# Performance work log

Measured on AMD Instinct MI355X. Metric: run time of the kernel, lower is better.

## Reference

```python
import jax, jax.numpy as jnp
import numpy as np

NGROUP, CIN, COUT, K, HIDDEN = 8, 16, 16, 5, True


def _build_mask():
    # Group-causal PixelCNN-style mask for a 5x5 kernel.
    # Spatial: rows above center fully visible; center row visible left of center.
    # Center tap: input group g_in visible to output group g_out iff
    #   g_in <= g_out (hidden layer) or g_in < g_out (input layer).
    nout, cinall = NGROUP * COUT, NGROUP * CIN
    c = K // 2
    m = np.zeros((nout, cinall, K, K), dtype=np.float32)
    m[:, :, :c, :] = 1.0          # rows strictly above center
    m[:, :, c, :c] = 1.0          # center row, left of center
    g_out = np.arange(nout)[:, None] // COUT   # (nout,1)
    g_in = np.arange(cinall)[None, :] // CIN   # (1,cinall)
    center_ok = (g_in <= g_out) if HIDDEN else (g_in < g_out)
    m[:, :, c, c] = center_ok.astype(np.float32)
    return jnp.asarray(m)

_MASK = _build_mask()


def setup_inputs() -> dict:
    key = jax.random.key(0)
    k1, k2 = jax.random.split(key)
    x = jax.random.normal(k1, (8, 128, 256, 512), dtype=jnp.float32)
    weight = jax.random.uniform(k2, (128, 128, 5, 5), dtype=jnp.float32)
    bias = jnp.zeros((128,), dtype=jnp.float32)
    slope = jnp.zeros((128,), dtype=jnp.float32)  # PReLU slope (zero -> ReLU)
    return {"x": x, "weight": weight, "bias": bias, "slope": slope}


def reference(x, weight, bias, slope):
    w = weight * _MASK  # apply causal group mask
    # context pad by 2 then valid 5x5 conv == SAME padding conv
    y = jax.lax.conv_general_dilated(
        x, w, window_strides=(1, 1), padding=((2, 2), (2, 2)),
        dimension_numbers=("NCHW", "OIHW", "NCHW"))
    y = y + bias[None, :, None, None]
    a = slope[None, :, None, None]
    return jnp.where(y > 0, y, a * y)  # per-channel PReLU
```

## Files before the change

kernel.cpp:

```cpp
#include <hip/hip_runtime.h>
#include <hip/hip_bf16.h>

typedef __attribute__((ext_vector_type(8))) short short8;
typedef __attribute__((ext_vector_type(4))) float f32x4;

#define CH 128
#define H 256
#define W 512
#define PH 258
#define PW 516
#define NTAPS 13
#define P_BYTES (PH * PW * CH * 2)
#define P_SHORTS (PH * PW * CH)
#define CHW (CH * H * W)

#define GRAN_PER_ROW 544
#define NLOADS 34
#define TILE_SHORTS (4 * GRAN_PER_ROW * 8)
#define ROW_SHORTS (GRAN_PER_ROW * 8)

#define GLD_LDS16(g, l)                                                        \
  __builtin_amdgcn_global_load_lds(                                            \
      (const __attribute__((address_space(1))) void*)(g),                      \
      (__attribute__((address_space(3))) void*)(l), 16, 0, 0)

__global__ void zero_pads(unsigned int* __restrict__ Pd) {
    int row  = blockIdx.x;
    int slab = blockIdx.y;
    unsigned int* base = Pd + (size_t)slab * (P_SHORTS / 2);
    int tid = threadIdx.x;
    if (row < 2) {
        unsigned int* r = base + (size_t)row * (PW * 64);
        for (int i = tid; i < PW * 64; i += 256) r[i] = 0u;
    } else {
        int seg = tid >> 6;
        int col = seg < 2 ? seg : 512 + seg;
        base[((size_t)row * PW + col) * 64 + (tid & 63)] = 0u;
    }
}

__global__ void premask_weights(const float* __restrict__ w,
                                __hip_bfloat16* __restrict__ Wt2) {
    int idx  = blockIdx.x * 256 + threadIdx.x;
    int frag = idx >> 9;
    int r    = idx & 511;
    int l    = r >> 3;
    int e    = r & 7;
    int t    = frag >> 5;
    int ob   = (frag >> 2) & 7;
    int kcg  = frag & 3;
    int oc   = ob * 16 + (l & 15);
    int ic   = kcg * 32 + (l >> 4) * 8 + e;
    int ky   = t < 5 ? 0 : (t < 10 ? 1 : 2);
    int kx   = t - ky * 5;
    float v  = w[(oc * CH + ic) * 25 + ky * 5 + kx];
    if (t == 12 && ((ic >> 4) > (oc >> 4))) v = 0.f;
    Wt2[idx] = __float2bfloat16(v);
}

__global__ void transpose_pad_all(const float* __restrict__ x,
                                  __hip_bfloat16* __restrict__ Pbase) {
    __shared__ float tile[32][33];
    const float* xn = x + (size_t)blockIdx.z * CHW;
    unsigned short* P = (unsigned short*)(Pbase + (size_t)blockIdx.z * P_SHORTS);
    int h  = blockIdx.y;
    int wt = blockIdx.x & 15;
    int ct = blockIdx.x >> 4;
    int tx = threadIdx.x & 31;
    int ty = threadIdx.x >> 5;
#pragma unroll
    for (int r = 0; r < 4; ++r) {
        int c = ct * 32 + ty + r * 8;
        tile[ty + r * 8][tx] = xn[(c * H + h) * W + wt * 32 + tx];
    }
    __syncthreads();
    int wl = threadIdx.x >> 3;
    int cq = threadIdx.x & 7;
    union { ushort4 u; __hip_bfloat16 hh[4]; } v;
    v.hh[0] = __float2bfloat16(tile[cq * 4 + 0][wl]);
    v.hh[1] = __float2bfloat16(tile[cq * 4 + 1][wl]);
    v.hh[2] = __float2bfloat16(tile[cq * 4 + 2][wl]);
    v.hh[3] = __float2bfloat16(tile[cq * 4 + 3][wl]);
    *reinterpret_cast<ushort4*>(
        P + ((size_t)(h + 2) * PW + (wt * 32 + wl + 2)) * CH + ct * 32 + cq * 4) = v.u;
}

__global__ __launch_bounds__(512, 4)
void conv_mfma_all(const __hip_bfloat16* __restrict__ Pbase,
                   const __hip_bfloat16* __restrict__ Wt2,
                   const float* __restrict__ bias,
                   const float* __restrict__ slope,
                   float* __restrict__ out) {
    __shared__ short lds[2 * TILE_SHORTS];
    const __hip_bfloat16* P = Pbase + (size_t)blockIdx.z * P_SHORTS;
    float* outn = out + (size_t)blockIdx.z * CHW;
    int h0   = blockIdx.y << 1;
    int w0   = blockIdx.x << 7;
    int tid  = threadIdx.x;
    int lane = tid & 63;
    int wv   = tid >> 6;
    int l15  = lane & 15;
    int khi  = lane >> 4;
    int ohf  = wv & 1;
    int pxh  = (wv >> 1) & 1;
    int hsel = wv >> 2;

    f32x4 acc[4][4];
#pragma unroll
    for (int mi = 0; mi < 4; ++mi)
#pragma unroll
        for (int ni = 0; ni < 4; ++ni)
            acc[mi][ni] = (f32x4){0.f, 0.f, 0.f, 0.f};

    const short* Wt2s = (const short*)Wt2;

    int stoff[5];
#pragma unroll
    for (int i = 0; i < 5; ++i) {
        int s    = wv + i * 8;
        int ss   = s < NLOADS ? s : NLOADS - 1;
        int g64  = (ss << 6) + lane;
        int row  = (g64 >= 544) + (g64 >= 1088) + (g64 >= 1632);
        int G    = g64 - row * GRAN_PER_ROW;
        int pair = G >> 3;
        int qd   = (G & 7) ^ (pair & 7);
        int px   = pair * 2 + (qd >> 2);
        int chk  = qd & 3;
        int pxc  = px < 132 ? px : 131;
        stoff[i] = ((h0 + row) * PW + (w0 + pxc)) * CH + chk * 8;
    }

    auto stage = [&](int kk, int bsel) {
#pragma unroll
        for (int i = 0; i < 5; ++i) {
            int s = wv + i * 8;
            if (s < NLOADS)
                GLD_LDS16(P + stoff[i] + kk * 32,
                          (char*)lds + bsel * (TILE_SHORTS * 2) + (s << 10));
        }
    };

    stage(0, 0);
    __syncthreads();

    for (int kk = 0; kk < 4; ++kk) {
        const int cur = kk & 1;
        if (kk < 3) stage(kk + 1, cur ^ 1);

        const short* bb = lds + cur * TILE_SHORTS + hsel * ROW_SHORTS;
#pragma unroll
        for (int t = 0; t < NTAPS; ++t) {
            const int ky = t < 5 ? 0 : (t < 10 ? 1 : 2);
            const int kx = t - ky * 5;
            const short* ap = Wt2s + ((t * 32 + ohf * 16 + kk) << 9) + (lane << 3);
            int p   = pxh * 64 + kx + l15;
            int pr  = p >> 1;
            int inr = (((p & 1) << 2) | khi) ^ (pr & 7);
            const short* bp = bb + ky * ROW_SHORTS + ((pr << 3) + inr) * 8;
            short8 a[4], b[4];
#pragma unroll
            for (int mi = 0; mi < 4; ++mi)
                a[mi] = *reinterpret_cast<const short8*>(ap + mi * 2048);
#pragma unroll
            for (int ni = 0; ni < 4; ++ni)
                b[ni] = *reinterpret_cast<const short8*>(bp + ni * 512);
            __builtin_amdgcn_s_setprio(1);
#pragma unroll
            for (int mi = 0; mi < 4; ++mi)
#pragma unroll
                for (int ni = 0; ni < 4; ++ni)
                    acc[mi][ni] = __builtin_amdgcn_mfma_f32_16x16x32_bf16(
                        a[mi], b[ni], acc[mi][ni], 0, 0, 0);
            __builtin_amdgcn_s_setprio(0);
        }
        __syncthreads();
    }

    int hrow = h0 + hsel;
#pragma unroll
    for (int mi = 0; mi < 4; ++mi) {
        int ocb = ohf * 64 + mi * 16 + 4 * khi;
        f32x4 b4 = *reinterpret_cast<const f32x4*>(bias + ocb);
        f32x4 s4 = *reinterpret_cast<const f32x4*>(slope + ocb);
#pragma unroll
        for (int i = 0; i < 4; ++i) {
            float* orow = outn + ((ocb + i) * H + hrow) * W + w0 + pxh * 64;
#pragma unroll
            for (int ni = 0; ni < 4; ++ni) {
                float v = acc[mi][ni][i] + b4[i];
                v = v > 0.f ? v : s4[i] * v;
                orow[ni * 16 + l15] = v;
            }
        }
    }
}

extern "C" void kernel_launch(void* const* d_in, const int* in_sizes, int n_in,
                              void* d_out, int out_size, void* d_ws, size_t ws_size,
                              hipStream_t stream) {
    const float* x      = (const float*)d_in[0];
    const float* weight = (const float*)d_in[1];
    const float* bias   = (const float*)d_in[2];
    const float* slope  = (const float*)d_in[3];
    float* out = (float*)d_out;

    __hip_bfloat16* Pbase = (__hip_bfloat16*)d_ws;
    __hip_bfloat16* Wt2   = (__hip_bfloat16*)((char*)d_ws + 8 * (size_t)P_BYTES);

    zero_pads<<<dim3(PH, 8), 256, 0, stream>>>((unsigned int*)d_ws);
    premask_weights<<<832, 256, 0, stream>>>(weight, Wt2);
    transpose_pad_all<<<dim3(64, 256, 8), 256, 0, stream>>>(x, Pbase);
    conv_mfma_all<<<dim3(4, 128, 8), 512, 0, stream>>>(Pbase, Wt2, bias, slope, out);
}
```

Baseline: 640.3 us.

## Load full-channel input tile once into LDS and remap blocks across XCDs

Replaces the four-stage double-buffered channel-chunk pipeline with a single bulk load of all 128 channels for the 4-row halo tile into LDS (about 139KB), then loops taps outer and channel chunks inner. One barrier replaces four, and the swizzle is redone for the wider rows. It also flattens the grid to 1D and remaps block ids so that each XCD gets a contiguous range of tiles, for better L2 locality. In exchange there is no overlap between global loads and MFMA inside a block, and occupancy drops to one or two blocks per CU because of the LDS size.

```diff
diff --git a/kernel.cpp b/kernel.cpp
--- a/kernel.cpp
+++ b/kernel.cpp
@@ -14,10 +14,9 @@
 #define P_SHORTS (PH * PW * CH)
 #define CHW (CH * H * W)
 
-#define GRAN_PER_ROW 544
-#define NLOADS 34
-#define TILE_SHORTS (4 * GRAN_PER_ROW * 8)
-#define ROW_SHORTS (GRAN_PER_ROW * 8)
+#define GRAN_PER_ROW 2176
+#define TOT_GRAN 8704
+#define NWLOADS 136
 
 #define GLD_LDS16(g, l)                                                        \
   __builtin_amdgcn_global_load_lds(                                            \
@@ -85,17 +84,22 @@
         P + ((size_t)(h + 2) * PW + (wt * 32 + wl + 2)) * CH + ct * 32 + cq * 4) = v.u;
 }
 
-__global__ __launch_bounds__(512, 4)
+__global__ __launch_bounds__(512, 2)
 void conv_mfma_all(const __hip_bfloat16* __restrict__ Pbase,
                    const __hip_bfloat16* __restrict__ Wt2,
                    const float* __restrict__ bias,
                    const float* __restrict__ slope,
                    float* __restrict__ out) {
-    __shared__ short lds[2 * TILE_SHORTS];
-    const __hip_bfloat16* P = Pbase + (size_t)blockIdx.z * P_SHORTS;
-    float* outn = out + (size_t)blockIdx.z * CHW;
-    int h0   = blockIdx.y << 1;
-    int w0   = blockIdx.x << 7;
+    __shared__ short lds[TOT_GRAN * 8];
+    int d   = blockIdx.x;
+    int lid = (d & 7) * 512 + (d >> 3);
+    int bz  = lid >> 9;
+    int by  = (lid >> 2) & 127;
+    int bx  = lid & 3;
+    const __hip_bfloat16* P = Pbase + (size_t)bz * P_SHORTS;
+    float* outn = out + (size_t)bz * CHW;
+    int h0   = by << 1;
+    int w0   = bx << 7;
     int tid  = threadIdx.x;
     int lane = tid & 63;
     int wv   = tid >> 6;
@@ -114,56 +118,40 @@
 
     const short* Wt2s = (const short*)Wt2;
 
-    int stoff[5];
-#pragma unroll
-    for (int i = 0; i < 5; ++i) {
+    for (int i = 0; i < 17; ++i) {
         int s    = wv + i * 8;
-        int ss   = s < NLOADS ? s : NLOADS - 1;
-        int g64  = (ss << 6) + lane;
-        int row  = (g64 >= 544) + (g64 >= 1088) + (g64 >= 1632);
-        int G    = g64 - row * GRAN_PER_ROW;
-        int pair = G >> 3;
-        int qd   = (G & 7) ^ (pair & 7);
-        int px   = pair * 2 + (qd >> 2);
-        int chk  = qd & 3;
+        int g    = (s << 6) + lane;
+        int row  = (g >= 2176) + (g >= 4352) + (g >= 6528);
+        int rem  = g - row * GRAN_PER_ROW;
+        int px   = rem >> 4;
+        int chk  = rem & 15;
         int pxc  = px < 132 ? px : 131;
-        stoff[i] = ((h0 + row) * PW + (w0 + pxc)) * CH + chk * 8;
-    }
-
-    auto stage = [&](int kk, int bsel) {
-#pragma unroll
-        for (int i = 0; i < 5; ++i) {
-            int s = wv + i * 8;
-            if (s < NLOADS)
-                GLD_LDS16(P + stoff[i] + kk * 32,
-                          (char*)lds + bsel * (TILE_SHORTS * 2) + (s << 10));
-        }
-    };
-
-    stage(0, 0);
+        int csrc = (chk & 8) | ((chk & 7) ^ (pxc & 7));
+        GLD_LDS16(P + ((h0 + row) * PW + (w0 + pxc)) * CH + csrc * 8,
+                  (char*)lds + (s << 10));
+    }
     __syncthreads();
 
-    for (int kk = 0; kk < 4; ++kk) {
-        const int cur = kk & 1;
-        if (kk < 3) stage(kk + 1, cur ^ 1);
-
-        const short* bb = lds + cur * TILE_SHORTS + hsel * ROW_SHORTS;
-#pragma unroll
-        for (int t = 0; t < NTAPS; ++t) {
-            const int ky = t < 5 ? 0 : (t < 10 ? 1 : 2);
-            const int kx = t - ky * 5;
-            const short* ap = Wt2s + ((t * 32 + ohf * 16 + kk) << 9) + (lane << 3);
-            int p   = pxh * 64 + kx + l15;
-            int pr  = p >> 1;
-            int inr = (((p & 1) << 2) | khi) ^ (pr & 7);
-            const short* bp = bb + ky * ROW_SHORTS + ((pr << 3) + inr) * 8;
+    int pbase = pxh * 64;
+    for (int t = 0; t < NTAPS; ++t) {
+        int ky = t < 5 ? 0 : (t < 10 ? 1 : 2);
+        int kx = t - ky * 5;
+        int p  = pbase + kx + l15;
+        int e  = p & 7;
+        const short* brow = lds + (((hsel + ky) * GRAN_PER_ROW + p * 16) << 3);
+        const short* apt  = Wt2s + (((t * 8 + ohf * 4) * 4) << 9) + (lane << 3);
+#pragma unroll
+        for (int kk = 0; kk < 4; ++kk) {
+            int csw = ((kk & 2) << 2) | ((((kk & 1) << 2) | khi) ^ e);
+            const short* bp = brow + (csw << 3);
+            const short* ap = apt + (kk << 9);
             short8 a[4], b[4];
 #pragma unroll
             for (int mi = 0; mi < 4; ++mi)
                 a[mi] = *reinterpret_cast<const short8*>(ap + mi * 2048);
 #pragma unroll
             for (int ni = 0; ni < 4; ++ni)
-                b[ni] = *reinterpret_cast<const short8*>(bp + ni * 512);
+                b[ni] = *reinterpret_cast<const short8*>(bp + ni * 2048);
             __builtin_amdgcn_s_setprio(1);
 #pragma unroll
             for (int mi = 0; mi < 4; ++mi)
@@ -173,7 +161,6 @@
                         a[mi], b[ni], acc[mi][ni], 0, 0, 0);
             __builtin_amdgcn_s_setprio(0);
         }
-        __syncthreads();
     }
 
     int hrow = h0 + hsel;
@@ -184,7 +171,7 @@
         f32x4 s4 = *reinterpret_cast<const f32x4*>(slope + ocb);
 #pragma unroll
         for (int i = 0; i < 4; ++i) {
-            float* orow = outn + ((ocb + i) * H + hrow) * W + w0 + pxh * 64;
+            float* orow = outn + ((ocb + i) * H + hrow) * W + w0 + pbase;
 #pragma unroll
             for (int ni = 0; ni < 4; ++ni) {
                 float v = acc[mi][ni][i] + b4[i];
@@ -210,5 +197,5 @@
     zero_pads<<<dim3(PH, 8), 256, 0, stream>>>((unsigned int*)d_ws);
     premask_weights<<<832, 256, 0, stream>>>(weight, Wt2);
     transpose_pad_all<<<dim3(64, 256, 8), 256, 0, stream>>>(x, Pbase);
-    conv_mfma_all<<<dim3(4, 128, 8), 512, 0, stream>>>(Pbase, Wt2, bias, slope, out);
-}
+    conv_mfma_all<<<4096, 512, 0, stream>>>(Pbase, Wt2, bias, slope, out);
+}
```

After: 678.9 us. 1.06x slower.
